# Kernel tuning notes

Hardware: AMD Instinct MI355X
Metric: run time of the kernel (lower is better)

Reference implementation:

```python
import jax, jax.numpy as jnp
import numpy as np

D_VISION = 1024
D_BRANCH = 256
N_BRANCHES = 4
N_HEADS = 4
HEAD_DIM = D_BRANCH // N_HEADS
DIVERSITY_WEIGHT = 0.1
LN_EPS = 1e-5


def setup_inputs() -> dict:
    key = jax.random.key(0)
    ks = jax.random.split(key, 8)
    B, T, N = 8, 16, 256
    frame_patches = jax.random.normal(ks[0], (B, T, N, D_VISION), dtype=jnp.float32)
    # LayerNorm params (shared input_norm)
    ln_gamma = jnp.ones((D_VISION,), jnp.float32)
    ln_beta = jnp.zeros((D_VISION,), jnp.float32)
    # Per-branch params stacked on a leading branch dim
    query = jax.random.normal(ks[1], (N_BRANCHES, N_HEADS, HEAD_DIM), jnp.float32) * 0.02
    wstd = 1.0 / np.sqrt(D_VISION)
    Wk = jax.random.uniform(ks[2], (N_BRANCHES, D_VISION, D_BRANCH), jnp.float32, -wstd, wstd)
    bk = jax.random.uniform(ks[3], (N_BRANCHES, D_BRANCH), jnp.float32, -wstd, wstd)
    Wv = jax.random.uniform(ks[4], (N_BRANCHES, D_VISION, D_BRANCH), jnp.float32, -wstd, wstd)
    bv = jax.random.uniform(ks[5], (N_BRANCHES, D_BRANCH), jnp.float32, -wstd, wstd)
    ostd = 1.0 / np.sqrt(D_BRANCH)
    Wo = jax.random.uniform(ks[6], (N_BRANCHES, D_BRANCH, D_BRANCH), jnp.float32, -ostd, ostd)
    bo = jax.random.uniform(ks[7], (N_BRANCHES, D_BRANCH), jnp.float32, -ostd, ostd)
    return dict(frame_patches=frame_patches, ln_gamma=ln_gamma, ln_beta=ln_beta,
                query=query, Wk=Wk, bk=bk, Wv=Wv, bv=bv, Wo=Wo, bo=bo)


def _layernorm(x, g, b):
    mu = jnp.mean(x, axis=-1, keepdims=True)
    var = jnp.var(x, axis=-1, keepdims=True)
    return (x - mu) * jax.lax.rsqrt(var + LN_EPS) * g + b


def reference(frame_patches, ln_gamma, ln_beta, query, Wk, bk, Wv, bv, Wo, bo):
    B, T, N, D = frame_patches.shape
    nb, H, hd = query.shape
    db = H * hd
    scale = hd ** -0.5
    x = _layernorm(frame_patches.reshape(B * T, N, D), ln_gamma, ln_beta)  # (BT, N, D)
    # Batched k/v projections across all branches (the fusion opportunity)
    k = (jnp.einsum('bpd,ndk->nbpk', x, Wk) + bk[:, None, None, :]).reshape(nb, B * T, N, H, hd)
    v = (jnp.einsum('bpd,ndk->nbpk', x, Wv) + bv[:, None, None, :]).reshape(nb, B * T, N, H, hd)
    # Single learnable query per (branch, head) attends over patches
    scores = jnp.einsum('nbphd,nhd->nbhp', k, query) * scale  # (nb, BT, H, N)
    attn = jax.nn.softmax(scores, axis=-1)
    attn_avg = attn.mean(axis=2)  # (nb, BT, N) head-averaged, pre-dropout
    # Dropout is inference no-op (eval mode)
    pooled = jnp.einsum('nbhp,nbphd->nbhd', attn, v).reshape(nb, B * T, db)
    out = jnp.einsum('nbk,nkj->nbj', pooled, Wo) + bo[:, None, :]  # (nb, BT, db)
    streams = out.transpose(1, 0, 2).reshape(B, T, nb, db)
    # Diversity loss: mean pairwise cosine similarity of attention distributions
    norms = jnp.maximum(jnp.linalg.norm(attn_avg, axis=-1, keepdims=True), 1e-8)
    a = attn_avg / norms
    sims = jnp.einsum('ibn,jbn->ijb', a, a).mean(axis=-1)  # (nb, nb)
    mask = jnp.triu(jnp.ones((nb, nb), attn_avg.dtype), k=1)
    diversity_loss = DIVERSITY_WEIGHT * (sims * mask).sum() / mask.sum()
    return streams, diversity_loss
```

## Files before the change

### kernel.cpp

```cpp
#include <hip/hip_runtime.h>
#include <stdint.h>

#define BT      128
#define NPATCH  256
#define DV      1024
#define NB      4
#define DB      256
#define NH16    16
#define SCALE   0.125f
#define LNEPS   1e-5f

#define OFF_GWQ    0u
#define OFF_BWS    16384u
#define OFF_S      24576u
#define OFF_CB     24592u
#define OFF_PSC    24608u
#define OFF_DRAW2  25120u
#define OFF_STATS2 1073696u
#define OFF_W      1204768u
#define OFF_CV     1729056u
#define OFF_DIV    1731104u
#define OFF_XBAR   1731872u
#define OFF_POOL   5926176u
#define XBAR_HALF  2097152u

typedef short bf16x8 __attribute__((ext_vector_type(8)));
typedef float f32x4  __attribute__((ext_vector_type(4)));

__device__ __forceinline__ short f2bf(float f) {
    union { float f; unsigned u; } v; v.f = f;
    unsigned u = v.u;
    unsigned r = (u + 0x7fffu + ((u >> 16) & 1u)) >> 16;
    return (short)r;
}

__device__ __forceinline__ unsigned pk2(float lo, float hi) {
    union { float f; unsigned u; } a, b; a.f = lo; b.f = hi;
    return __builtin_amdgcn_perm(b.u, a.u, 0x07060302u);
}

__global__ __launch_bounds__(256) void kP(const float* __restrict__ Wk,
                                          const float* __restrict__ q,
                                          const float* __restrict__ g,
                                          const float* __restrict__ b,
                                          float* __restrict__ ws) {
    const int nh = blockIdx.x >> 4, ich = blockIdx.x & 15;
    const int n = nh >> 2, h = nh & 3;
    __shared__ float qs[64];
    __shared__ float redS[4], redC[4];
    const int t = threadIdx.x;
    if (t < 64) qs[t] = q[nh * 64 + t];
    __syncthreads();
    const int r = t >> 2, qd = t & 3;
    const int i = ich * 64 + r;
    const float* wrow = Wk + ((size_t)n * DV + i) * DB + h * 64 + qd * 16;
    float acc = 0.f;
    #pragma unroll
    for (int d = 0; d < 16; d += 4) {
        float4 w4 = *(const float4*)(wrow + d);
        acc += w4.x * qs[qd * 16 + d]     + w4.y * qs[qd * 16 + d + 1]
             + w4.z * qs[qd * 16 + d + 2] + w4.w * qs[qd * 16 + d + 3];
    }
    acc += __shfl_xor(acc, 1);
    acc += __shfl_xor(acc, 2);
    float gw = g[i] * acc;
    if (qd == 0) ws[OFF_GWQ + nh * DV + i] = gw;
    float mS = (qd == 0) ? gw : 0.f;
    float mC = (qd == 0) ? b[i] * acc : 0.f;
    #pragma unroll
    for (int dd = 4; dd < 64; dd <<= 1) { mS += __shfl_xor(mS, dd); mC += __shfl_xor(mC, dd); }
    const int wave = t >> 6, lane = t & 63;
    if (lane == 0) { redS[wave] = mS; redC[wave] = mC; }
    __syncthreads();
    if (t == 0) {
        ws[OFF_PSC + (nh * 16 + ich) * 2 + 0] = redS[0] + redS[1] + redS[2] + redS[3];
        ws[OFF_PSC + (nh * 16 + ich) * 2 + 1] = redC[0] + redC[1] + redC[2] + redC[3];
    }
}

__global__ __launch_bounds__(1024) void kP2(const float* __restrict__ q,
                                            const float* __restrict__ bk,
                                            float* __restrict__ ws) {
    const int blk = blockIdx.x;
    const int t = threadIdx.x;
    if (blk == 16) {
        if (t < 16) {
            const int nh = t, n = nh >> 2, h = nh & 3;
            float S = 0.f, C = 0.f;
            for (int ich = 0; ich < 16; ++ich) {
                S += ws[OFF_PSC + (nh * 16 + ich) * 2 + 0];
                C += ws[OFF_PSC + (nh * 16 + ich) * 2 + 1];
            }
            float bkq = 0.f;
            for (int d = 0; d < 64; ++d) bkq += bk[n * DB + h * 64 + d] * q[nh * 64 + d];
            ws[OFF_S + nh]  = S;
            ws[OFF_CB + nh] = C + bkq;
        }
        return;
    }
    unsigned short* bws = (unsigned short*)(ws + OFF_BWS);
    const float* gwq = ws + OFF_GWQ;
    const int idx = blk * 1024 + t;
    const int j = idx & 7, lane = (idx >> 3) & 63, kt = idx >> 9;
    const int nh = lane & 15;
    const int k = kt * 32 + ((lane >> 4) * 8) + j;
    bws[idx] = (unsigned short)f2bf(gwq[nh * DV + k]);
}

__global__ __launch_bounds__(256) void kA(const float* __restrict__ x,
                                          float* __restrict__ ws) {
    const int t = threadIdx.x;
    const int wave = t >> 6, lane = t & 63;
    const int task = blockIdx.x * 4 + wave;
    const int khalf = task & 1, tile = task >> 1;
    const int m = lane & 15, oct = lane >> 4;
    const int row0 = tile * 16;
    const float* xrow = x + (size_t)(row0 + m) * DV + khalf * 512 + oct * 8;
    const bf16x8* bfp = (const bf16x8*)((const unsigned short*)(ws + OFF_BWS)) + khalf * 1024;

    f32x4 acc = {0.f, 0.f, 0.f, 0.f};
    float sum = 0.f, sq = 0.f;
    #pragma unroll 4
    for (int kt = 0; kt < 16; ++kt) {
        float4 a0 = *(const float4*)(xrow + kt * 32);
        float4 a1 = *(const float4*)(xrow + kt * 32 + 4);
        union { bf16x8 v; unsigned w[4]; } af;
        af.w[0] = pk2(a0.x, a0.y); af.w[1] = pk2(a0.z, a0.w);
        af.w[2] = pk2(a1.x, a1.y); af.w[3] = pk2(a1.z, a1.w);
        bf16x8 bfr = bfp[kt * 64 + lane];
        acc = __builtin_amdgcn_mfma_f32_16x16x32_bf16(af.v, bfr, acc, 0, 0, 0);
        sum += a0.x + a0.y + a0.z + a0.w + a1.x + a1.y + a1.z + a1.w;
        sq  += a0.x * a0.x + a0.y * a0.y + a0.z * a0.z + a0.w * a0.w
             + a1.x * a1.x + a1.y * a1.y + a1.z * a1.z + a1.w * a1.w;
    }
    sum += __shfl_xor(sum, 16); sum += __shfl_xor(sum, 32);
    sq  += __shfl_xor(sq, 16);  sq  += __shfl_xor(sq, 32);
    if (lane < 16) {
        ws[OFF_STATS2 + (size_t)khalf * 65536 + (size_t)(row0 + lane) * 2 + 0] = sum;
        ws[OFF_STATS2 + (size_t)khalf * 65536 + (size_t)(row0 + lane) * 2 + 1] = sq;
    }
    #pragma unroll
    for (int r = 0; r < 4; ++r)
        ws[OFF_DRAW2 + (size_t)khalf * 524288 + (size_t)(row0 + oct * 4 + r) * 16 + m] = acc[r];
}

__global__ __launch_bounds__(256) void kB(float* __restrict__ ws) {
    const int bt = blockIdx.x;
    const int t = threadIdx.x;
    __shared__ __attribute__((aligned(16))) float s_s[NH16 * NPATCH];
    __shared__ __attribute__((aligned(16))) float aavg[NB * NPATCH];
    __shared__ __attribute__((aligned(16))) float rstd_s[NPATCH];
    __shared__ __attribute__((aligned(16))) float mrs[NPATCH];
    __shared__ float Ss[NH16], Cbs[NH16];
    if (t < NH16) Ss[t] = ws[OFF_S + t];
    else if (t < 32) Cbs[t - 16] = ws[OFF_CB + (t - 16)];
    const size_t row = (size_t)bt * NPATCH + t;
    const float sum = ws[OFF_STATS2 + row * 2 + 0] + ws[OFF_STATS2 + 65536 + row * 2 + 0];
    const float sq  = ws[OFF_STATS2 + row * 2 + 1] + ws[OFF_STATS2 + 65536 + row * 2 + 1];
    const float mu   = sum * (1.f / 1024.f);
    const float var  = sq * (1.f / 1024.f) - mu * mu;
    const float rstd = rsqrtf(var + LNEPS);
    rstd_s[t] = rstd;
    mrs[t] = mu * rstd;
    __syncthreads();
    const float* dr0 = ws + OFF_DRAW2 + row * 16;
    const float* dr1 = dr0 + 524288;
    #pragma unroll
    for (int nh = 0; nh < NH16; ++nh) {
        float D = dr0[nh] + dr1[nh];
        s_s[nh * NPATCH + t] = (rstd * (D - mu * Ss[nh]) + Cbs[nh]) * SCALE;
    }
    __syncthreads();
    const int wave = t >> 6, lane = t & 63;
    for (int r = 0; r < 4; ++r) {
        const int nh = wave * 4 + r;
        float4 v = *(float4*)&s_s[nh * NPATCH + lane * 4];
        float mx = fmaxf(fmaxf(v.x, v.y), fmaxf(v.z, v.w));
        for (int d = 1; d < 64; d <<= 1) mx = fmaxf(mx, __shfl_xor(mx, d));
        float e0 = __expf(v.x - mx), e1 = __expf(v.y - mx);
        float e2 = __expf(v.z - mx), e3 = __expf(v.w - mx);
        float s = e0 + e1 + e2 + e3;
        for (int d = 1; d < 64; d <<= 1) s += __shfl_xor(s, d);
        float inv = 1.f / s;
        float4 a; a.x = e0 * inv; a.y = e1 * inv; a.z = e2 * inv; a.w = e3 * inv;
        *(float4*)&s_s[nh * NPATCH + lane * 4] = a;
        float4 r4 = *(float4*)&rstd_s[lane * 4];
        float4 wv; wv.x = a.x * r4.x; wv.y = a.y * r4.y; wv.z = a.z * r4.z; wv.w = a.w * r4.w;
        *(float4*)(ws + OFF_W + (size_t)(bt * NH16 + nh) * NPATCH + lane * 4) = wv;
    }
    __syncthreads();
    for (int r = 0; r < 4; ++r) {
        const int nh = wave * 4 + r;
        float4 a4 = *(float4*)&s_s[nh * NPATCH + lane * 4];
        float4 m4 = *(float4*)&mrs[lane * 4];
        float dd = a4.x * m4.x + a4.y * m4.y + a4.z * m4.z + a4.w * m4.w;
        for (int d = 1; d < 64; d <<= 1) dd += __shfl_xor(dd, d);
        if (lane == 0) ws[OFF_CV + bt * NH16 + nh] = dd;
    }
    #pragma unroll
    for (int n = 0; n < NB; ++n)
        aavg[n * NPATCH + t] = 0.25f * (s_s[(n * 4 + 0) * NPATCH + t] + s_s[(n * 4 + 1) * NPATCH + t]
                                      + s_s[(n * 4 + 2) * NPATCH + t] + s_s[(n * 4 + 3) * NPATCH + t]);
    __syncthreads();
    if (wave == 0) {
        float nrm[NB];
        #pragma unroll
        for (int n = 0; n < NB; ++n) {
            float4 v = *(float4*)&aavg[n * NPATCH + lane * 4];
            float ss = v.x * v.x + v.y * v.y + v.z * v.z + v.w * v.w;
            for (int d = 1; d < 64; d <<= 1) ss += __shfl_xor(ss, d);
            nrm[n] = fmaxf(sqrtf(ss), 1e-8f);
        }
        int pi = 0;
        for (int i = 0; i < NB; ++i)
            for (int j = i + 1; j < NB; ++j) {
                float4 va = *(float4*)&aavg[i * NPATCH + lane * 4];
                float4 vb = *(float4*)&aavg[j * NPATCH + lane * 4];
                float dd = va.x * vb.x + va.y * vb.y + va.z * vb.z + va.w * vb.w;
                for (int d = 1; d < 64; d <<= 1) dd += __shfl_xor(dd, d);
                if (lane == 0) ws[OFF_DIV + bt * 6 + pi] = dd / (nrm[i] * nrm[j]);
                ++pi;
            }
    }
}

__global__ __launch_bounds__(512) void kC(const float* __restrict__ x,
                                          float* __restrict__ ws) {
    const int bt = blockIdx.x;
    const int half = blockIdx.y;
    const int t = threadIdx.x;
    __shared__ __attribute__((aligned(16))) float w_s[128 * 16];
    for (int idx = t; idx < 2048; idx += 512) {
        int p = idx >> 4, nh = idx & 15;
        w_s[idx] = ws[OFF_W + (size_t)(bt * NH16 + nh) * NPATCH + half * 128 + p];
    }
    float2 acc[16];
    #pragma unroll
    for (int i = 0; i < 16; ++i) { acc[i].x = 0.f; acc[i].y = 0.f; }
    __syncthreads();
    const float* xp = x + (size_t)(bt * NPATCH + half * 128) * DV + t * 2;
    #pragma unroll 8
    for (int p = 0; p < 128; ++p) {
        float2 xv = *(const float2*)(xp + (size_t)p * DV);
        float4 a0 = *(const float4*)&w_s[p * 16 + 0];
        float4 a1 = *(const float4*)&w_s[p * 16 + 4];
        float4 a2 = *(const float4*)&w_s[p * 16 + 8];
        float4 a3 = *(const float4*)&w_s[p * 16 + 12];
        acc[0].x  += a0.x * xv.x; acc[0].y  += a0.x * xv.y;
        acc[1].x  += a0.y * xv.x; acc[1].y  += a0.y * xv.y;
        acc[2].x  += a0.z * xv.x; acc[2].y  += a0.z * xv.y;
        acc[3].x  += a0.w * xv.x; acc[3].y  += a0.w * xv.y;
        acc[4].x  += a1.x * xv.x; acc[4].y  += a1.x * xv.y;
        acc[5].x  += a1.y * xv.x; acc[5].y  += a1.y * xv.y;
        acc[6].x  += a1.z * xv.x; acc[6].y  += a1.z * xv.y;
        acc[7].x  += a1.w * xv.x; acc[7].y  += a1.w * xv.y;
        acc[8].x  += a2.x * xv.x; acc[8].y  += a2.x * xv.y;
        acc[9].x  += a2.y * xv.x; acc[9].y  += a2.y * xv.y;
        acc[10].x += a2.z * xv.x; acc[10].y += a2.z * xv.y;
        acc[11].x += a2.w * xv.x; acc[11].y += a2.w * xv.y;
        acc[12].x += a3.x * xv.x; acc[12].y += a3.x * xv.y;
        acc[13].x += a3.y * xv.x; acc[13].y += a3.y * xv.y;
        acc[14].x += a3.z * xv.x; acc[14].y += a3.z * xv.y;
        acc[15].x += a3.w * xv.x; acc[15].y += a3.w * xv.y;
    }
    #pragma unroll
    for (int nh = 0; nh < 16; ++nh)
        *(float2*)(ws + OFF_XBAR + (size_t)half * XBAR_HALF
                   + ((size_t)bt * NH16 + nh) * DV + t * 2) = acc[nh];
}

__global__ __launch_bounds__(256) void kD1(const float* __restrict__ Wv,
                                           const float* __restrict__ g,
                                           const float* __restrict__ b,
                                           const float* __restrict__ bv,
                                           float* __restrict__ ws) {
    const int nh = blockIdx.x & 15, btg = blockIdx.x >> 4;
    const int n = nh >> 2, h = nh & 3;
    const int bt0 = btg * 8, cb = h * 64;
    __shared__ __attribute__((aligned(16))) float xs[8][1024];
    __shared__ __attribute__((aligned(16))) float gs[1024], bs[1024];
    __shared__ float red[4][64][10];
    const int t = threadIdx.x;
    for (int e = t; e < 2048; e += 256) {
        const int bt = e >> 8, i4 = e & 255;
        const size_t b0 = OFF_XBAR + ((size_t)(bt0 + bt) * NH16 + nh) * DV + i4 * 4;
        float4 v0 = *(const float4*)(ws + b0);
        float4 v1 = *(const float4*)(ws + b0 + XBAR_HALF);
        float4 s; s.x = v0.x + v1.x; s.y = v0.y + v1.y; s.z = v0.z + v1.z; s.w = v0.w + v1.w;
        *(float4*)&xs[bt][i4 * 4] = s;
    }
    for (int e = t; e < 1024; e += 256) { gs[e] = g[e]; bs[e] = b[e]; }
    __syncthreads();
    const int c = t & 63, sub = t >> 6;
    float acc[8];
    #pragma unroll
    for (int l = 0; l < 8; ++l) acc[l] = 0.f;
    float gv = 0.f, bvv = 0.f;
    const float* wvp = Wv + ((size_t)n * DV + sub * 256) * DB + cb + c;
    const int ib0 = sub * 256;
    #pragma unroll 2
    for (int gidx = 0; gidx < 64; ++gidx) {
        const int ib = ib0 + gidx * 4;
        float w0 = wvp[(size_t)(gidx * 4 + 0) * DB];
        float w1 = wvp[(size_t)(gidx * 4 + 1) * DB];
        float w2 = wvp[(size_t)(gidx * 4 + 2) * DB];
        float w3 = wvp[(size_t)(gidx * 4 + 3) * DB];
        float4 g4 = *(const float4*)&gs[ib];
        float4 b4 = *(const float4*)&bs[ib];
        float q0 = g4.x * w0, q1 = g4.y * w1, q2 = g4.z * w2, q3 = g4.w * w3;
        gv  += q0 + q1 + q2 + q3;
        bvv += b4.x * w0 + b4.y * w1 + b4.z * w2 + b4.w * w3;
        #pragma unroll
        for (int l = 0; l < 8; ++l) {
            float4 xr = *(const float4*)&xs[l][ib];
            acc[l] += xr.x * q0 + xr.y * q1 + xr.z * q2 + xr.w * q3;
        }
    }
    #pragma unroll
    for (int l = 0; l < 8; ++l) red[sub][c][l] = acc[l];
    red[sub][c][8] = gv; red[sub][c][9] = bvv;
    __syncthreads();
    const int c2 = t & 63, l0 = t >> 6;
    float gvS = red[0][c2][8] + red[1][c2][8] + red[2][c2][8] + red[3][c2][8];
    float bvS = red[0][c2][9] + red[1][c2][9] + red[2][c2][9] + red[3][c2][9];
    float base = bv[n * DB + cb + c2] + bvS;
    #pragma unroll
    for (int li = 0; li < 2; ++li) {
        const int l = l0 + li * 4;
        float p = red[0][c2][l] + red[1][c2][l] + red[2][c2][l] + red[3][c2][l];
        float C = ws[OFF_CV + (bt0 + l) * NH16 + nh];
        ws[OFF_POOL + ((size_t)n * BT + bt0 + l) * DB + cb + c2] = p - C * gvS + base;
    }
}

__global__ __launch_bounds__(256) void kD2(const float* __restrict__ Wo,
                                           const float* __restrict__ bo,
                                           const float* __restrict__ ws,
                                           float* __restrict__ out) {
    const int btg = blockIdx.x & 15, jq = (blockIdx.x >> 4) & 3, n = blockIdx.x >> 6;
    const int bt0 = btg * 8, j0 = jq * 64;
    __shared__ __attribute__((aligned(16))) float ps[8][256];
    __shared__ float red[4][64][8];
    const int t = threadIdx.x;
    for (int e = t; e < 512; e += 256) {
        const int bt = e >> 6, c4 = e & 63;
        *(float4*)&ps[bt][c4 * 4] =
            *(const float4*)(ws + OFF_POOL + ((size_t)n * BT + bt0 + bt) * DB + c4 * 4);
    }
    __syncthreads();
    const int j = t & 63, sub = t >> 6;
    float acc[8];
    #pragma unroll
    for (int l = 0; l < 8; ++l) acc[l] = 0.f;
    const float* wop = Wo + ((size_t)n * DB + sub * 64) * DB + j0 + j;
    const int cb0 = sub * 64;
    #pragma unroll 2
    for (int gidx = 0; gidx < 16; ++gidx) {
        const int cb = cb0 + gidx * 4;
        float w0 = wop[(size_t)(gidx * 4 + 0) * DB];
        float w1 = wop[(size_t)(gidx * 4 + 1) * DB];
        float w2 = wop[(size_t)(gidx * 4 + 2) * DB];
        float w3 = wop[(size_t)(gidx * 4 + 3) * DB];
        #pragma unroll
        for (int l = 0; l < 8; ++l) {
            float4 pr = *(const float4*)&ps[l][cb];
            acc[l] += pr.x * w0 + pr.y * w1 + pr.z * w2 + pr.w * w3;
        }
    }
    #pragma unroll
    for (int l = 0; l < 8; ++l) red[sub][j][l] = acc[l];
    __syncthreads();
    const int j2 = t & 63, l0 = t >> 6;
    float bov = bo[n * DB + j0 + j2];
    #pragma unroll
    for (int li = 0; li < 2; ++li) {
        const int l = l0 + li * 4;
        float o = red[0][j2][l] + red[1][j2][l] + red[2][j2][l] + red[3][j2][l] + bov;
        out[((size_t)(bt0 + l) * NB + n) * DB + j0 + j2] = o;
    }
}

__global__ __launch_bounds__(256) void kE(const float* __restrict__ ws,
                                          float* __restrict__ out) {
    const int t = threadIdx.x;
    float acc = 0.f;
    for (int idx = t; idx < 768; idx += 256) acc += ws[OFF_DIV + idx];
    __shared__ float red[4];
    for (int d = 1; d < 64; d <<= 1) acc += __shfl_xor(acc, d);
    if ((t & 63) == 0) red[t >> 6] = acc;
    __syncthreads();
    if (t == 0) out[131072] = 0.1f * (red[0] + red[1] + red[2] + red[3]) / (6.f * 128.f);
}

extern "C" void kernel_launch(void* const* d_in, const int* in_sizes, int n_in,
                              void* d_out, int out_size, void* d_ws, size_t ws_size,
                              hipStream_t stream) {
    const float* x  = (const float*)d_in[0];
    const float* g  = (const float*)d_in[1];
    const float* b  = (const float*)d_in[2];
    const float* q  = (const float*)d_in[3];
    const float* Wk = (const float*)d_in[4];
    const float* bk = (const float*)d_in[5];
    const float* Wv = (const float*)d_in[6];
    const float* bv = (const float*)d_in[7];
    const float* Wo = (const float*)d_in[8];
    const float* bo = (const float*)d_in[9];
    float* out = (float*)d_out;
    float* ws  = (float*)d_ws;

    hipLaunchKernelGGL(kP,  dim3(256),    dim3(256),  0, stream, Wk, q, g, b, ws);
    hipLaunchKernelGGL(kP2, dim3(17),     dim3(1024), 0, stream, q, bk, ws);
    hipLaunchKernelGGL(kA,  dim3(1024),   dim3(256),  0, stream, x, ws);
    hipLaunchKernelGGL(kB,  dim3(128),    dim3(256),  0, stream, ws);
    hipLaunchKernelGGL(kC,  dim3(128, 2), dim3(512),  0, stream, x, ws);
    hipLaunchKernelGGL(kD1, dim3(256),    dim3(256),  0, stream, Wv, g, b, bv, ws);
    hipLaunchKernelGGL(kD2, dim3(256),    dim3(256),  0, stream, Wo, bo, ws, out);
    hipLaunchKernelGGL(kE,  dim3(1),      dim3(256),  0, stream, ws, out);
}
```

Before: 291.8 us.

## Stage x through LDS in kA, split kC over four patch quarters, fold kE

```diff
diff --git a/kernel.cpp b/kernel.cpp
--- a/kernel.cpp
+++ b/kernel.cpp
@@ -15,14 +15,16 @@
 #define OFF_S      24576u
 #define OFF_CB     24592u
 #define OFF_PSC    24608u
-#define OFF_DRAW2  25120u
-#define OFF_STATS2 1073696u
-#define OFF_W      1204768u
-#define OFF_CV     1729056u
-#define OFF_DIV    1731104u
-#define OFF_XBAR   1731872u
-#define OFF_POOL   5926176u
-#define XBAR_HALF  2097152u
+#define OFF_DRAW   25120u
+#define OFF_STATS  549408u
+#define OFF_W      614944u
+#define OFF_CV     1139232u
+#define OFF_DIV    1141280u
+#define OFF_XBAR   1142048u
+#define OFF_POOL   9530656u
+#define XSLICE     2097152u
+
+#define LROW 264
 
 typedef short bf16x8 __attribute__((ext_vector_type(8)));
 typedef float f32x4  __attribute__((ext_vector_type(4)));
@@ -109,39 +111,65 @@
 
 __global__ __launch_bounds__(256) void kA(const float* __restrict__ x,
                                           float* __restrict__ ws) {
-    const int t = threadIdx.x;
-    const int wave = t >> 6, lane = t & 63;
-    const int task = blockIdx.x * 4 + wave;
-    const int khalf = task & 1, tile = task >> 1;
+    __shared__ unsigned short xs[2][64 * LROW];
+    const int t = threadIdx.x;
+    const int wv = t >> 6, lane = t & 63;
     const int m = lane & 15, oct = lane >> 4;
-    const int row0 = tile * 16;
-    const float* xrow = x + (size_t)(row0 + m) * DV + khalf * 512 + oct * 8;
-    const bf16x8* bfp = (const bf16x8*)((const unsigned short*)(ws + OFF_BWS)) + khalf * 1024;
-
+    const int row0 = blockIdx.x * 64;
+    const bf16x8* bfp = (const bf16x8*)((const unsigned short*)(ws + OFF_BWS));
+    const float* xb = x + (size_t)row0 * DV;
+
+    float sum[16], sq[16];
+    #pragma unroll
+    for (int i = 0; i < 16; ++i) { sum[i] = 0.f; sq[i] = 0.f; }
     f32x4 acc = {0.f, 0.f, 0.f, 0.f};
-    float sum = 0.f, sq = 0.f;
-    #pragma unroll 4
-    for (int kt = 0; kt < 16; ++kt) {
-        float4 a0 = *(const float4*)(xrow + kt * 32);
-        float4 a1 = *(const float4*)(xrow + kt * 32 + 4);
-        union { bf16x8 v; unsigned w[4]; } af;
-        af.w[0] = pk2(a0.x, a0.y); af.w[1] = pk2(a0.z, a0.w);
-        af.w[2] = pk2(a1.x, a1.y); af.w[3] = pk2(a1.z, a1.w);
-        bf16x8 bfr = bfp[kt * 64 + lane];
-        acc = __builtin_amdgcn_mfma_f32_16x16x32_bf16(af.v, bfr, acc, 0, 0, 0);
-        sum += a0.x + a0.y + a0.z + a0.w + a1.x + a1.y + a1.z + a1.w;
-        sq  += a0.x * a0.x + a0.y * a0.y + a0.z * a0.z + a0.w * a0.w
-             + a1.x * a1.x + a1.y * a1.y + a1.z * a1.z + a1.w * a1.w;
-    }
-    sum += __shfl_xor(sum, 16); sum += __shfl_xor(sum, 32);
-    sq  += __shfl_xor(sq, 16);  sq  += __shfl_xor(sq, 32);
-    if (lane < 16) {
-        ws[OFF_STATS2 + (size_t)khalf * 65536 + (size_t)(row0 + lane) * 2 + 0] = sum;
-        ws[OFF_STATS2 + (size_t)khalf * 65536 + (size_t)(row0 + lane) * 2 + 1] = sq;
-    }
+
+    auto stage = [&](int c, int buf) {
+        #pragma unroll
+        for (int i = 0; i < 16; ++i) {
+            const int row = i * 4 + wv;
+            float4 v = *(const float4*)(xb + (size_t)row * DV + c * 256 + lane * 4);
+            sum[i] += v.x + v.y + v.z + v.w;
+            sq[i]  += v.x * v.x + v.y * v.y + v.z * v.z + v.w * v.w;
+            uint2 pk; pk.x = pk2(v.x, v.y); pk.y = pk2(v.z, v.w);
+            *(uint2*)&xs[buf][row * LROW + lane * 4] = pk;
+        }
+    };
+    auto comp = [&](int c, int buf) {
+        #pragma unroll
+        for (int kt = 0; kt < 8; ++kt) {
+            bf16x8 af = *(const bf16x8*)&xs[buf][(wv * 16 + m) * LROW + kt * 32 + oct * 8];
+            bf16x8 bf = bfp[(c * 8 + kt) * 64 + lane];
+            acc = __builtin_amdgcn_mfma_f32_16x16x32_bf16(af, bf, acc, 0, 0, 0);
+        }
+    };
+
+    stage(0, 0);
+    __syncthreads();
+    #pragma unroll
+    for (int c = 0; c < 4; ++c) {
+        if (c < 3) stage(c + 1, (c + 1) & 1);
+        comp(c, c & 1);
+        __syncthreads();
+    }
+
     #pragma unroll
     for (int r = 0; r < 4; ++r)
-        ws[OFF_DRAW2 + (size_t)khalf * 524288 + (size_t)(row0 + oct * 4 + r) * 16 + m] = acc[r];
+        ws[OFF_DRAW + (size_t)(row0 + wv * 16 + oct * 4 + r) * 16 + m] = acc[r];
+
+    #pragma unroll
+    for (int i = 0; i < 16; ++i) {
+        float s = sum[i], q2 = sq[i];
+        #pragma unroll
+        for (int d = 1; d < 64; d <<= 1) { s += __shfl_xor(s, d); q2 += __shfl_xor(q2, d); }
+        if (lane == 0) {
+            const int row = row0 + i * 4 + wv;
+            const float mu  = s * (1.f / 1024.f);
+            const float var = q2 * (1.f / 1024.f) - mu * mu;
+            float2 st; st.x = mu; st.y = rsqrtf(var + LNEPS);
+            *(float2*)(ws + OFF_STATS + (size_t)row * 2) = st;
+        }
+    }
 }
 
 __global__ __launch_bounds__(256) void kB(float* __restrict__ ws) {
@@ -155,19 +183,15 @@
     if (t < NH16) Ss[t] = ws[OFF_S + t];
     else if (t < 32) Cbs[t - 16] = ws[OFF_CB + (t - 16)];
     const size_t row = (size_t)bt * NPATCH + t;
-    const float sum = ws[OFF_STATS2 + row * 2 + 0] + ws[OFF_STATS2 + 65536 + row * 2 + 0];
-    const float sq  = ws[OFF_STATS2 + row * 2 + 1] + ws[OFF_STATS2 + 65536 + row * 2 + 1];
-    const float mu   = sum * (1.f / 1024.f);
-    const float var  = sq * (1.f / 1024.f) - mu * mu;
-    const float rstd = rsqrtf(var + LNEPS);
+    const float2 st = *(const float2*)(ws + OFF_STATS + row * 2);
+    const float mu = st.x, rstd = st.y;
     rstd_s[t] = rstd;
     mrs[t] = mu * rstd;
     __syncthreads();
-    const float* dr0 = ws + OFF_DRAW2 + row * 16;
-    const float* dr1 = dr0 + 524288;
+    const float* dr = ws + OFF_DRAW + row * 16;
     #pragma unroll
     for (int nh = 0; nh < NH16; ++nh) {
-        float D = dr0[nh] + dr1[nh];
+        float D = dr[nh];
         s_s[nh * NPATCH + t] = (rstd * (D - mu * Ss[nh]) + Cbs[nh]) * SCALE;
     }
     __syncthreads();
@@ -224,49 +248,40 @@
     }
 }
 
-__global__ __launch_bounds__(512) void kC(const float* __restrict__ x,
+__global__ __launch_bounds__(256) void kC(const float* __restrict__ x,
                                           float* __restrict__ ws) {
     const int bt = blockIdx.x;
-    const int half = blockIdx.y;
-    const int t = threadIdx.x;
-    __shared__ __attribute__((aligned(16))) float w_s[128 * 16];
-    for (int idx = t; idx < 2048; idx += 512) {
+    const int qq = blockIdx.y;
+    const int t = threadIdx.x;
+    __shared__ __attribute__((aligned(16))) float w_s[64 * 16];
+    for (int idx = t; idx < 1024; idx += 256) {
         int p = idx >> 4, nh = idx & 15;
-        w_s[idx] = ws[OFF_W + (size_t)(bt * NH16 + nh) * NPATCH + half * 128 + p];
-    }
-    float2 acc[16];
-    #pragma unroll
-    for (int i = 0; i < 16; ++i) { acc[i].x = 0.f; acc[i].y = 0.f; }
-    __syncthreads();
-    const float* xp = x + (size_t)(bt * NPATCH + half * 128) * DV + t * 2;
-    #pragma unroll 8
-    for (int p = 0; p < 128; ++p) {
-        float2 xv = *(const float2*)(xp + (size_t)p * DV);
+        w_s[idx] = ws[OFF_W + (size_t)(bt * NH16 + nh) * NPATCH + qq * 64 + p];
+    }
+    float4 acc[16];
+    #pragma unroll
+    for (int i = 0; i < 16; ++i) { acc[i].x = 0.f; acc[i].y = 0.f; acc[i].z = 0.f; acc[i].w = 0.f; }
+    __syncthreads();
+    const float* xp = x + (size_t)(bt * NPATCH + qq * 64) * DV + t * 4;
+    #pragma unroll 4
+    for (int p = 0; p < 64; ++p) {
+        float4 xv = *(const float4*)(xp + (size_t)p * DV);
         float4 a0 = *(const float4*)&w_s[p * 16 + 0];
         float4 a1 = *(const float4*)&w_s[p * 16 + 4];
         float4 a2 = *(const float4*)&w_s[p * 16 + 8];
         float4 a3 = *(const float4*)&w_s[p * 16 + 12];
-        acc[0].x  += a0.x * xv.x; acc[0].y  += a0.x * xv.y;
-        acc[1].x  += a0.y * xv.x; acc[1].y  += a0.y * xv.y;
-        acc[2].x  += a0.z * xv.x; acc[2].y  += a0.z * xv.y;
-        acc[3].x  += a0.w * xv.x; acc[3].y  += a0.w * xv.y;
-        acc[4].x  += a1.x * xv.x; acc[4].y  += a1.x * xv.y;
-        acc[5].x  += a1.y * xv.x; acc[5].y  += a1.y * xv.y;
-        acc[6].x  += a1.z * xv.x; acc[6].y  += a1.z * xv.y;
-        acc[7].x  += a1.w * xv.x; acc[7].y  += a1.w * xv.y;
-        acc[8].x  += a2.x * xv.x; acc[8].y  += a2.x * xv.y;
-        acc[9].x  += a2.y * xv.x; acc[9].y  += a2.y * xv.y;
-        acc[10].x += a2.z * xv.x; acc[10].y += a2.z * xv.y;
-        acc[11].x += a2.w * xv.x; acc[11].y += a2.w * xv.y;
-        acc[12].x += a3.x * xv.x; acc[12].y += a3.x * xv.y;
-        acc[13].x += a3.y * xv.x; acc[13].y += a3.y * xv.y;
-        acc[14].x += a3.z * xv.x; acc[14].y += a3.z * xv.y;
-        acc[15].x += a3.w * xv.x; acc[15].y += a3.w * xv.y;
+        #define FMA4(k, wgt) acc[k].x += (wgt) * xv.x; acc[k].y += (wgt) * xv.y; \
+                             acc[k].z += (wgt) * xv.z; acc[k].w += (wgt) * xv.w;
+        FMA4(0, a0.x)  FMA4(1, a0.y)  FMA4(2, a0.z)  FMA4(3, a0.w)
+        FMA4(4, a1.x)  FMA4(5, a1.y)  FMA4(6, a1.z)  FMA4(7, a1.w)
+        FMA4(8, a2.x)  FMA4(9, a2.y)  FMA4(10, a2.z) FMA4(11, a2.w)
+        FMA4(12, a3.x) FMA4(13, a3.y) FMA4(14, a3.z) FMA4(15, a3.w)
+        #undef FMA4
     }
     #pragma unroll
     for (int nh = 0; nh < 16; ++nh)
-        *(float2*)(ws + OFF_XBAR + (size_t)half * XBAR_HALF
-                   + ((size_t)bt * NH16 + nh) * DV + t * 2) = acc[nh];
+        *(float4*)(ws + OFF_XBAR + (size_t)qq * XSLICE
+                   + ((size_t)bt * NH16 + nh) * DV + t * 4) = acc[nh];
 }
 
 __global__ __launch_bounds__(256) void kD1(const float* __restrict__ Wv,
@@ -284,9 +299,12 @@
     for (int e = t; e < 2048; e += 256) {
         const int bt = e >> 8, i4 = e & 255;
         const size_t b0 = OFF_XBAR + ((size_t)(bt0 + bt) * NH16 + nh) * DV + i4 * 4;
-        float4 v0 = *(const float4*)(ws + b0);
-        float4 v1 = *(const float4*)(ws + b0 + XBAR_HALF);
-        float4 s; s.x = v0.x + v1.x; s.y = v0.y + v1.y; s.z = v0.z + v1.z; s.w = v0.w + v1.w;
+        float4 s = {0.f, 0.f, 0.f, 0.f};
+        #pragma unroll
+        for (int qq = 0; qq < 4; ++qq) {
+            float4 v = *(const float4*)(ws + b0 + (size_t)qq * XSLICE);
+            s.x += v.x; s.y += v.y; s.z += v.z; s.w += v.w;
+        }
         *(float4*)&xs[bt][i4 * 4] = s;
     }
     for (int e = t; e < 1024; e += 256) { gs[e] = g[e]; bs[e] = b[e]; }
@@ -341,13 +359,21 @@
     const int bt0 = btg * 8, j0 = jq * 64;
     __shared__ __attribute__((aligned(16))) float ps[8][256];
     __shared__ float red[4][64][8];
+    __shared__ float dred[4];
     const int t = threadIdx.x;
     for (int e = t; e < 512; e += 256) {
         const int bt = e >> 6, c4 = e & 63;
         *(float4*)&ps[bt][c4 * 4] =
             *(const float4*)(ws + OFF_POOL + ((size_t)n * BT + bt0 + bt) * DB + c4 * 4);
     }
-    __syncthreads();
+    float dacc = 0.f;
+    if (blockIdx.x == 0)
+        for (int idx = t; idx < 768; idx += 256) dacc += ws[OFF_DIV + idx];
+    for (int d = 1; d < 64; d <<= 1) dacc += __shfl_xor(dacc, d);
+    if ((t & 63) == 0) dred[t >> 6] = dacc;
+    __syncthreads();
+    if (blockIdx.x == 0 && t == 0)
+        out[131072] = 0.1f * (dred[0] + dred[1] + dred[2] + dred[3]) / 768.f;
     const int j = t & 63, sub = t >> 6;
     float acc[8];
     #pragma unroll
@@ -378,18 +404,6 @@
         float o = red[0][j2][l] + red[1][j2][l] + red[2][j2][l] + red[3][j2][l] + bov;
         out[((size_t)(bt0 + l) * NB + n) * DB + j0 + j2] = o;
     }
-}
-
-__global__ __launch_bounds__(256) void kE(const float* __restrict__ ws,
-                                          float* __restrict__ out) {
-    const int t = threadIdx.x;
-    float acc = 0.f;
-    for (int idx = t; idx < 768; idx += 256) acc += ws[OFF_DIV + idx];
-    __shared__ float red[4];
-    for (int d = 1; d < 64; d <<= 1) acc += __shfl_xor(acc, d);
-    if ((t & 63) == 0) red[t >> 6] = acc;
-    __syncthreads();
-    if (t == 0) out[131072] = 0.1f * (red[0] + red[1] + red[2] + red[3]) / (6.f * 128.f);
 }
 
 extern "C" void kernel_launch(void* const* d_in, const int* in_sizes, int n_in,
@@ -410,10 +424,9 @@
 
     hipLaunchKernelGGL(kP,  dim3(256),    dim3(256),  0, stream, Wk, q, g, b, ws);
     hipLaunchKernelGGL(kP2, dim3(17),     dim3(1024), 0, stream, q, bk, ws);
-    hipLaunchKernelGGL(kA,  dim3(1024),   dim3(256),  0, stream, x, ws);
+    hipLaunchKernelGGL(kA,  dim3(512),    dim3(256),  0, stream, x, ws);
     hipLaunchKernelGGL(kB,  dim3(128),    dim3(256),  0, stream, ws);
-    hipLaunchKernelGGL(kC,  dim3(128, 2), dim3(512),  0, stream, x, ws);
+    hipLaunchKernelGGL(kC,  dim3(128, 4), dim3(256),  0, stream, x, ws);
     hipLaunchKernelGGL(kD1, dim3(256),    dim3(256),  0, stream, Wv, g, b, bv, ws);
     hipLaunchKernelGGL(kD2, dim3(256),    dim3(256),  0, stream, Wo, bo, ws, out);
-    hipLaunchKernelGGL(kE,  dim3(1),      dim3(256),  0, stream, ws, out);
-}
+}
```

Measured after the change: 302.5 us. +3.6%, slower.
